# Optimization experiments

Hardware: AMD Instinct MI355X
Metric: run time of the kernel (lower is better)

The kernel has to match this reference:

```python
import jax, jax.numpy as jnp
import numpy as np
import math

# --- config (matches init_kwargs) ---
C = 128          # sphere_channels (multiplicity per l)
LMAX = 2
H = 8            # attention heads
B = 16           # graphs per batch (uniform)
M = 512          # nodes per graph
N = B * M        # 8192 nodes
E = 262144       # edges
D = C * sum(2 * l + 1 for l in range(LMAX + 1))  # 1152
_INV_SQRT_C = 1.0 / math.sqrt(C)


def irreps_linear(x, W):
    """e3nn o3.Linear irreps_node->irreps_node: per-l channel mixing, shared over m.
    x: [N, D], W: [LMAX+1, C, C]."""
    outs = []
    s = 0
    for l in range(LMAX + 1):
        d = 2 * l + 1
        blk = x[:, s:s + C * d].reshape(-1, C, d)          # [N, C, 2l+1]
        y = jnp.einsum('ncm,oc->nom', blk, W[l]) * _INV_SQRT_C
        outs.append(y.reshape(-1, C * d))
        s += C * d
    return jnp.concatenate(outs, axis=1)


def init_edge_rot_mat(edge_vec, edge_rand):
    """Faithful port of init_edge_rot_mat; edge_rand plays the role of rand_like."""
    dist = jnp.sqrt(jnp.sum(edge_vec ** 2, axis=1, keepdims=True))
    nx_ = edge_vec / dist
    e2 = edge_rand - 0.5
    e2 = e2 / jnp.sqrt(jnp.sum(e2 ** 2, axis=1, keepdims=True))
    e2b = jnp.stack([-e2[:, 1], e2[:, 0], e2[:, 2]], axis=1)
    e2c = jnp.stack([e2[:, 0], -e2[:, 2], e2[:, 1]], axis=1)
    dot = lambda a: jnp.abs(jnp.sum(a * nx_, axis=1, keepdims=True))
    vdb, vdc = dot(e2b), dot(e2c)
    e2 = jnp.where(dot(e2) > vdb, e2b, e2)
    e2 = jnp.where(dot(e2) > vdc, e2c, e2)
    nz = jnp.cross(nx_, e2)
    nz = nz / jnp.sqrt(jnp.sum(nz ** 2, axis=1, keepdims=True))
    ny = jnp.cross(nx_, nz)
    ny = ny / jnp.sqrt(jnp.sum(ny ** 2, axis=1, keepdims=True))
    rot_inv = jnp.stack([nz, nx_, -ny], axis=2)  # columns [z, x, -y]
    return jnp.transpose(rot_inv, (0, 2, 1))     # [E, 3, 3]


def setup_inputs() -> dict:
    key = jax.random.key(0)
    ks = jax.random.split(key, 10)
    node_features = jax.random.normal(ks[0], (N, D), dtype=jnp.float32)
    edge_vec = jax.random.normal(ks[1], (E, 3), dtype=jnp.float32)
    edge_rand = jax.random.uniform(ks[2], (E, 3), dtype=jnp.float32)
    edge_index = jax.random.randint(ks[3], (2, E), 0, N, dtype=jnp.int32)
    batch = jnp.repeat(jnp.arange(B, dtype=jnp.int32), M)
    W_q = jax.random.normal(ks[4], (LMAX + 1, C, C), dtype=jnp.float32)
    W_k = jax.random.normal(ks[5], (LMAX + 1, C, C), dtype=jnp.float32)
    W_v = jax.random.normal(ks[6], (LMAX + 1, C, C), dtype=jnp.float32)
    W_o = jax.random.normal(ks[7], (LMAX + 1, C, C), dtype=jnp.float32)
    gamma = jnp.ones((C,), dtype=jnp.float32)
    beta = jnp.zeros((C,), dtype=jnp.float32)
    return dict(node_features=node_features, edge_vec=edge_vec, edge_rand=edge_rand,
                W_q=W_q, W_k=W_k, W_v=W_v, W_o=W_o, gamma=gamma, beta=beta,
                edge_index=edge_index, batch=batch)


def reference(node_features, edge_vec, edge_rand, W_q, W_k, W_v, W_o, gamma, beta,
              edge_index, batch):
    # 1) per-edge rotation matrices (detached in the original)
    rot = jax.lax.stop_gradient(init_edge_rot_mat(edge_vec, edge_rand))

    x = node_features  # [N, D] equivariant irreps features

    # 2) SO2EquivariantGraphAttention: irreps q/k/v, dense per-graph multi-head attn
    q = irreps_linear(x, W_q)
    k = irreps_linear(x, W_k)
    v = irreps_linear(x, W_v)
    hd = D // H
    scale = 1.0 / math.sqrt(hd)
    # to_dense_batch with uniform graph sizes == reshape; mask all-true
    qd = q.reshape(B, M, H, hd).transpose(0, 2, 1, 3)  # [B,H,M,hd]
    kd = k.reshape(B, M, H, hd).transpose(0, 2, 1, 3)
    vd = v.reshape(B, M, H, hd).transpose(0, 2, 1, 3)
    scores = jnp.einsum('bhqd,bhkd->bhqk', qd, kd) * scale
    attn_w = jax.nn.softmax(scores, axis=-1)
    o = jnp.einsum('bhqk,bhkd->bhqd', attn_w, vd)
    o = o.transpose(0, 2, 1, 3).reshape(N, D)
    attn_out = irreps_linear(o, W_o)

    # residual connection
    x = x + attn_out

    # 3) EquivariantLayerNormV2: LayerNorm over l=0 dims only (first C)
    inv = x[:, :C]
    mu = jnp.mean(inv, axis=-1, keepdims=True)
    var = jnp.var(inv, axis=-1, keepdims=True)
    inv = (inv - mu) / jnp.sqrt(var + 1e-5) * gamma + beta

    # 4) S2Activation: SiLU on scalar (l=0) components, identity elsewhere
    inv = jax.nn.silu(inv)
    out = jnp.concatenate([inv, x[:, C:]], axis=1)
    return out, rot
```

## Files before the change

kernel.cpp:

```cpp
#include <hip/hip_runtime.h>
#include <hip/hip_bf16.h>

#define C_CH   128
#define DROW   1152
#define NNODE  8192
#define BATCH  16
#define MSEQ   512
#define NHEAD  8
#define HD     144
#define NEDGE  262144

typedef unsigned short ushort_t;
typedef __attribute__((ext_vector_type(8))) short bf16x8;
typedef __attribute__((ext_vector_type(4))) float f32x4;

__device__ __forceinline__ ushort_t f2bu(float x) {
    __hip_bfloat16 h = __float2bfloat16(x);
    return *reinterpret_cast<ushort_t*>(&h);
}
__device__ __forceinline__ float bu2f(ushort_t u) {
    return __bfloat162float(*reinterpret_cast<__hip_bfloat16*>(&u));
}
__device__ __forceinline__ unsigned u16of(const uint4 v, int ii) {
    const unsigned w = ((ii >> 1) == 0) ? v.x : ((ii >> 1) == 1) ? v.y :
                       ((ii >> 1) == 2) ? v.z : v.w;
    return (ii & 1) ? (w >> 16) : (w & 0xFFFFu);
}

#define KP2 136

template<int DL, int NPB, typename TX, typename TY>
__global__ __launch_bounds__(256) void lin_ovl(
    const TX* __restrict__ X,
    const float* __restrict__ W0, const float* __restrict__ W1,
    const float* __restrict__ W2,
    TY* __restrict__ Y0, TY* __restrict__ Y1, TY* __restrict__ Y2,
    const float* __restrict__ resid,
    int baseoff)
{
    constexpr int COLS = NPB * DL;
    constexpr int CT   = COLS / 16;
    __shared__ __align__(16) ushort_t Bs[COLS][KP2];

    const int tid  = threadIdx.x;
    const int wave = tid >> 6;
    const int lane = tid & 63;
    const int l15  = lane & 15;
    const int quad = lane >> 4;
    const int n0   = blockIdx.x * NPB;
    const int z    = blockIdx.y;

    const float* W = (z == 0) ? W0 : (z == 1 ? W1 : W2);
    TY* Y          = (z == 0) ? Y0 : (z == 1 ? Y1 : Y2);

    if constexpr (sizeof(TX) == 4) {
        for (int e4 = tid; e4 < NPB * 32 * DL; e4 += 256) {
            const int nb = e4 / (32 * DL);
            const int rr = (e4 - nb * (32 * DL)) * 4;
            const float4 xv = *reinterpret_cast<const float4*>(
                &X[(size_t)(n0 + nb) * DROW + baseoff + rr]);
            #pragma unroll
            for (int j = 0; j < 4; ++j) {
                const int r = rr + j, c = r / DL, m = r - c * DL;
                Bs[nb * DL + m][c] = f2bu(reinterpret_cast<const float*>(&xv)[j]);
            }
        }
    } else {
        for (int e8 = tid; e8 < NPB * 16 * DL; e8 += 256) {
            const int nb = e8 / (16 * DL);
            const int rr = (e8 - nb * (16 * DL)) * 8;
            const uint4 xv = *reinterpret_cast<const uint4*>(
                &X[(size_t)(n0 + nb) * DROW + baseoff + rr]);
            const ushort_t* xs = reinterpret_cast<const ushort_t*>(&xv);
            #pragma unroll
            for (int j = 0; j < 8; ++j) {
                const int r = rr + j, c = r / DL, m = r - c * DL;
                Bs[nb * DL + m][c] = xs[j];
            }
        }
    }

    const float s = 0.08838834764831845f;

    bf16x8 aw[2][4];
    #pragma unroll
    for (int ot = 0; ot < 2; ++ot)
        #pragma unroll
        for (int kst = 0; kst < 4; ++kst) {
            const float* wp = &W[(size_t)(32 * wave + 16 * ot + l15) * 128 + kst * 32 + quad * 8];
            const float4 wa = *reinterpret_cast<const float4*>(wp);
            const float4 wb = *reinterpret_cast<const float4*>(wp + 4);
            ushort_t t[8] = {f2bu(wa.x), f2bu(wa.y), f2bu(wa.z), f2bu(wa.w),
                             f2bu(wb.x), f2bu(wb.y), f2bu(wb.z), f2bu(wb.w)};
            aw[ot][kst] = *reinterpret_cast<const bf16x8*>(t);
        }

    __syncthreads();

    f32x4 acc[CT][2];
    #pragma unroll
    for (int ct = 0; ct < CT; ++ct) {
        acc[ct][0] = (f32x4){0.f, 0.f, 0.f, 0.f};
        acc[ct][1] = (f32x4){0.f, 0.f, 0.f, 0.f};
    }
    #pragma unroll
    for (int kst = 0; kst < 4; ++kst)
        #pragma unroll
        for (int ct = 0; ct < CT; ++ct) {
            const bf16x8 b = *reinterpret_cast<const bf16x8*>(
                &Bs[ct * 16 + l15][kst * 32 + quad * 8]);
            acc[ct][0] = __builtin_amdgcn_mfma_f32_16x16x32_bf16(aw[0][kst], b, acc[ct][0], 0, 0, 0);
            acc[ct][1] = __builtin_amdgcn_mfma_f32_16x16x32_bf16(aw[1][kst], b, acc[ct][1], 0, 0, 0);
        }

    __syncthreads();

    #pragma unroll
    for (int ct = 0; ct < CT; ++ct)
        #pragma unroll
        for (int ot = 0; ot < 2; ++ot) {
            ushort_t t[4] = {f2bu(acc[ct][ot][0] * s), f2bu(acc[ct][ot][1] * s),
                             f2bu(acc[ct][ot][2] * s), f2bu(acc[ct][ot][3] * s)};
            *reinterpret_cast<uint2*>(&Bs[ct * 16 + l15][32 * wave + 16 * ot + quad * 4]) =
                *reinterpret_cast<const uint2*>(t);
        }
    __syncthreads();

    for (int e8 = tid; e8 < COLS * 16; e8 += 256) {
        const int nb = e8 / (16 * DL);
        const int r0 = (e8 - nb * (16 * DL)) * 8;
        const size_t ga = (size_t)(n0 + nb) * DROW + baseoff + r0;
        if constexpr (sizeof(TY) == 2) {
            ushort_t t[8];
            #pragma unroll
            for (int j = 0; j < 8; ++j) {
                const int r = r0 + j;
                t[j] = Bs[nb * DL + r % DL][r / DL];
            }
            *reinterpret_cast<uint4*>(&Y[ga]) = *reinterpret_cast<const uint4*>(t);
        } else {
            #pragma unroll
            for (int j4 = 0; j4 < 2; ++j4) {
                const float4 rv = *reinterpret_cast<const float4*>(&resid[ga + j4 * 4]);
                float4 ov;
                #pragma unroll
                for (int j = 0; j < 4; ++j) {
                    const int r = r0 + j4 * 4 + j;
                    reinterpret_cast<float*>(&ov)[j] =
                        bu2f(Bs[nb * DL + r % DL][r / DL]) +
                        reinterpret_cast<const float*>(&rv)[j];
                }
                *reinterpret_cast<float4*>(&((float*)Y)[ga + j4 * 4]) = ov;
            }
        }
    }
}

template<int DL, int NPB, int NZ, int FUSE_LN, typename TX, typename TY>
__global__ __launch_bounds__(256) void lin_mfma(
    const TX* __restrict__ X,
    const float* __restrict__ W0, const float* __restrict__ W1,
    const float* __restrict__ W2,
    TY* __restrict__ Y0, TY* __restrict__ Y1, TY* __restrict__ Y2,
    const float* __restrict__ resid,
    const float* __restrict__ gamma, const float* __restrict__ beta,
    int baseoff)
{
    constexpr int COLS = NPB * DL;
    constexpr int CT   = COLS / 16;
    __shared__ __align__(16) ushort_t Xs[COLS][KP2];
    __shared__ __align__(16) ushort_t Es[COLS][KP2];

    const int tid  = threadIdx.x;
    const int wave = tid >> 6;
    const int lane = tid & 63;
    const int l15  = lane & 15;
    const int quad = lane >> 4;
    const int n0   = blockIdx.x * NPB;

    if constexpr (sizeof(TX) == 4) {
        for (int e4 = tid; e4 < NPB * 32 * DL; e4 += 256) {
            const int nb = e4 / (32 * DL);
            const int rr = (e4 - nb * (32 * DL)) * 4;
            const float4 xv = *reinterpret_cast<const float4*>(
                &X[(size_t)(n0 + nb) * DROW + baseoff + rr]);
            #pragma unroll
            for (int j = 0; j < 4; ++j) {
                const int r = rr + j, c = r / DL, m = r - c * DL;
                Xs[nb * DL + m][c] = f2bu(reinterpret_cast<const float*>(&xv)[j]);
            }
        }
    } else {
        for (int e8 = tid; e8 < NPB * 16 * DL; e8 += 256) {
            const int nb = e8 / (16 * DL);
            const int rr = (e8 - nb * (16 * DL)) * 8;
            const uint4 xv = *reinterpret_cast<const uint4*>(
                &X[(size_t)(n0 + nb) * DROW + baseoff + rr]);
            const ushort_t* xs = reinterpret_cast<const ushort_t*>(&xv);
            #pragma unroll
            for (int j = 0; j < 8; ++j) {
                const int r = rr + j, c = r / DL, m = r - c * DL;
                Xs[nb * DL + m][c] = xs[j];
            }
        }
    }

    const float s = 0.08838834764831845f;

    for (int z = 0; z < NZ; ++z) {
        const float* W = (z == 0) ? W0 : (z == 1 ? W1 : W2);
        TY* Y          = (z == 0) ? Y0 : (z == 1 ? Y1 : Y2);

        bf16x8 aw[2][4];
        #pragma unroll
        for (int ot = 0; ot < 2; ++ot)
            #pragma unroll
            for (int kst = 0; kst < 4; ++kst) {
                const float* wp = &W[(size_t)(32 * wave + 16 * ot + l15) * 128 + kst * 32 + quad * 8];
                const float4 wa = *reinterpret_cast<const float4*>(wp);
                const float4 wb = *reinterpret_cast<const float4*>(wp + 4);
                ushort_t t[8] = {f2bu(wa.x), f2bu(wa.y), f2bu(wa.z), f2bu(wa.w),
                                 f2bu(wb.x), f2bu(wb.y), f2bu(wb.z), f2bu(wb.w)};
                aw[ot][kst] = *reinterpret_cast<const bf16x8*>(t);
            }

        __syncthreads();

        f32x4 acc[CT][2];
        #pragma unroll
        for (int ct = 0; ct < CT; ++ct) {
            acc[ct][0] = (f32x4){0.f, 0.f, 0.f, 0.f};
            acc[ct][1] = (f32x4){0.f, 0.f, 0.f, 0.f};
        }
        #pragma unroll
        for (int kst = 0; kst < 4; ++kst)
            #pragma unroll
            for (int ct = 0; ct < CT; ++ct) {
                const bf16x8 b = *reinterpret_cast<const bf16x8*>(
                    &Xs[ct * 16 + l15][kst * 32 + quad * 8]);
                acc[ct][0] = __builtin_amdgcn_mfma_f32_16x16x32_bf16(aw[0][kst], b, acc[ct][0], 0, 0, 0);
                acc[ct][1] = __builtin_amdgcn_mfma_f32_16x16x32_bf16(aw[1][kst], b, acc[ct][1], 0, 0, 0);
            }

        #pragma unroll
        for (int ct = 0; ct < CT; ++ct)
            #pragma unroll
            for (int ot = 0; ot < 2; ++ot) {
                ushort_t t[4] = {f2bu(acc[ct][ot][0] * s), f2bu(acc[ct][ot][1] * s),
                                 f2bu(acc[ct][ot][2] * s), f2bu(acc[ct][ot][3] * s)};
                *reinterpret_cast<uint2*>(&Es[ct * 16 + l15][32 * wave + 16 * ot + quad * 4]) =
                    *reinterpret_cast<const uint2*>(t);
            }
        __syncthreads();

        if constexpr (FUSE_LN) {
            if (tid < NPB * 4) {
                const int nb = tid >> 2, cc = tid & 3;
                float y[32];
                const float* xr = resid + (size_t)(n0 + nb) * DROW + cc * 32;
                float s1 = 0.f, s2 = 0.f;
                #pragma unroll
                for (int j4 = 0; j4 < 8; ++j4) {
                    const float4 rv = *reinterpret_cast<const float4*>(xr + j4 * 4);
                    #pragma unroll
                    for (int j = 0; j < 4; ++j) {
                        const float v = bu2f(Es[nb][cc * 32 + j4 * 4 + j]) +
                                        reinterpret_cast<const float*>(&rv)[j];
                        y[j4 * 4 + j] = v; s1 += v; s2 += v * v;
                    }
                }
                s1 += __shfl_xor(s1, 1); s2 += __shfl_xor(s2, 1);
                s1 += __shfl_xor(s1, 2); s2 += __shfl_xor(s2, 2);
                const float mean = s1 * (1.0f / 128.0f);
                const float var  = s2 * (1.0f / 128.0f) - mean * mean;
                const float rstd = rsqrtf(var + 1e-5f);
                float* op = (float*)Y + (size_t)(n0 + nb) * DROW + cc * 32;
                #pragma unroll
                for (int j4 = 0; j4 < 8; ++j4) {
                    float4 ov;
                    #pragma unroll
                    for (int j = 0; j < 4; ++j) {
                        const int c = cc * 32 + j4 * 4 + j;
                        float t = (y[j4 * 4 + j] - mean) * rstd * gamma[c] + beta[c];
                        reinterpret_cast<float*>(&ov)[j] = t / (1.0f + __expf(-t));
                    }
                    *reinterpret_cast<float4*>(op + j4 * 4) = ov;
                }
            }
        } else {
            for (int e8 = tid; e8 < COLS * 16; e8 += 256) {
                const int nb = e8 / (16 * DL);
                const int r0 = (e8 - nb * (16 * DL)) * 8;
                const size_t ga = (size_t)(n0 + nb) * DROW + baseoff + r0;
                if constexpr (sizeof(TY) == 2) {
                    ushort_t t[8];
                    #pragma unroll
                    for (int j = 0; j < 8; ++j) {
                        const int r = r0 + j;
                        t[j] = Es[nb * DL + r % DL][r / DL];
                    }
                    *reinterpret_cast<uint4*>(&Y[ga]) = *reinterpret_cast<const uint4*>(t);
                } else {
                    #pragma unroll
                    for (int j4 = 0; j4 < 2; ++j4) {
                        const float4 rv = *reinterpret_cast<const float4*>(&resid[ga + j4 * 4]);
                        float4 ov;
                        #pragma unroll
                        for (int j = 0; j < 4; ++j) {
                            const int r = r0 + j4 * 4 + j;
                            reinterpret_cast<float*>(&ov)[j] =
                                bu2f(Es[nb * DL + r % DL][r / DL]) +
                                reinterpret_cast<const float*>(&rv)[j];
                        }
                        *reinterpret_cast<float4*>(&((float*)Y)[ga + j4 * 4]) = ov;
                    }
                }
            }
        }
    }
}

#define KPAD  168
#define VROWS 160
#define VPAD2 72
#define PPAD  68

__global__ __launch_bounds__(256, 2) void attn_kernel(
    const __hip_bfloat16* __restrict__ Q, const __hip_bfloat16* __restrict__ K,
    const __hip_bfloat16* __restrict__ V, __hip_bfloat16* __restrict__ O)
{
    __shared__ __align__(16) ushort_t ksqs[64][KPAD];
    __shared__ __align__(16) ushort_t vst[VROWS][VPAD2];
    __shared__ __align__(16) ushort_t ps[128][PPAD];

    const int tid  = threadIdx.x;
    const int wave = tid >> 6;
    const int lane = tid & 63;
    const int l15  = lane & 15;
    const int quad = lane >> 4;

    const int bid = blockIdx.x;
    const int xcd = bid & 7;
    const int j   = bid >> 3;
    const int bh  = xcd * 16 + (j >> 2);
    const int q0  = (j & 3) * 128;
    const int h   = bh & 7;
    const int b   = bh >> 3;
    const size_t rowbase = (size_t)b * MSEQ * DROW + (size_t)h * HD;
    const float EXSCALE = 0.12022458674074695f;

    const int r0 = tid / 18,          g0 = tid % 18;
    const int r1 = (tid + 256) / 18,  g1 = (tid + 256) % 18;
    const int r2 = (tid + 512) / 18,  g2 = (tid + 512) % 18;
    const int r3 = (tid + 768) / 18,  g3 = (tid + 768) % 18;
    const int r4 = (tid + 1024) / 18, g4 = (tid + 1024) % 18;
    const int ko0 = r0 * DROW + g0 * 8, ko1 = r1 * DROW + g1 * 8;
    const int ko2 = r2 * DROW + g2 * 8, ko3 = r3 * DROW + g3 * 8;
    const int ko4 = r4 * DROW + g4 * 8;
    ushort_t* kld0 = &ksqs[r0][g0 * 8];
    ushort_t* kld1 = &ksqs[r1][g1 * 8];
    ushort_t* kld2 = &ksqs[r2][g2 * 8];
    ushort_t* kld3 = &ksqs[r3][g3 * 8];
    ushort_t* kld4 = &ksqs[r4][g4 * 8];
    const int rqa = tid / 18,          ga = tid % 18;
    const int rqb = (tid + 256) / 18,  gb = (tid + 256) % 18;
    const int voa = (rqa * 4) * DROW + ga * 8;
    const int vob = (rqb * 4) * DROW + gb * 8;
    const int vca = 4 * (rqa ^ ((ga & 3) << 2));
    const int vcb = 4 * (rqb ^ ((gb & 3) << 2));
    const bool hasK4 = (tid < 128);
    const bool hasVB = (tid < 32);

    uint4 kp0, kp1, kp2, kp3, kp4;
    uint4 va0, va1, va2, va3, vb0, vb1, vb2, vb3;

#define LOAD_K(KC) do { \
        const __hip_bfloat16* kb_ = K + rowbase + (size_t)((KC) * 64) * DROW; \
        kp0 = *reinterpret_cast<const uint4*>(kb_ + ko0); \
        kp1 = *reinterpret_cast<const uint4*>(kb_ + ko1); \
        kp2 = *reinterpret_cast<const uint4*>(kb_ + ko2); \
        kp3 = *reinterpret_cast<const uint4*>(kb_ + ko3); \
        if (hasK4) kp4 = *reinterpret_cast<const uint4*>(kb_ + ko4); \
    } while (0)

#define LOAD_V(KC) do { \
        const __hip_bfloat16* vbp_ = V + rowbase + (size_t)((KC) * 64) * DROW; \
        va0 = *reinterpret_cast<const uint4*>(vbp_ + voa); \
        va1 = *reinterpret_cast<const uint4*>(vbp_ + voa + DROW); \
        va2 = *reinterpret_cast<const uint4*>(vbp_ + voa + 2 * DROW); \
        va3 = *reinterpret_cast<const uint4*>(vbp_ + voa + 3 * DROW); \
        if (hasVB) { \
            vb0 = *reinterpret_cast<const uint4*>(vbp_ + vob); \
            vb1 = *reinterpret_cast<const uint4*>(vbp_ + vob + DROW); \
            vb2 = *reinterpret_cast<const uint4*>(vbp_ + vob + 2 * DROW); \
            vb3 = *reinterpret_cast<const uint4*>(vbp_ + vob + 3 * DROW); \
        } \
    } while (0)

#define WRITE_KV() do { \
        *reinterpret_cast<uint4*>(kld0) = kp0; \
        *reinterpret_cast<uint4*>(kld1) = kp1; \
        *reinterpret_cast<uint4*>(kld2) = kp2; \
        *reinterpret_cast<uint4*>(kld3) = kp3; \
        if (hasK4) *reinterpret_cast<uint4*>(kld4) = kp4; \
        _Pragma("unroll") \
        for (int ii = 0; ii < 8; ++ii) { \
            uint2 pk; \
            pk.x = u16of(va0, ii) | (u16of(va1, ii) << 16); \
            pk.y = u16of(va2, ii) | (u16of(va3, ii) << 16); \
            *reinterpret_cast<uint2*>(&vst[ga * 8 + ii][vca]) = pk; \
        } \
        if (hasVB) { \
            _Pragma("unroll") \
            for (int ii = 0; ii < 8; ++ii) { \
                uint2 pk; \
                pk.x = u16of(vb0, ii) | (u16of(vb1, ii) << 16); \
                pk.y = u16of(vb2, ii) | (u16of(vb3, ii) << 16); \
                *reinterpret_cast<uint2*>(&vst[gb * 8 + ii][vcb]) = pk; \
            } \
        } \
    } while (0)

    LOAD_K(0);
    LOAD_V(0);

    for (int idx = tid; idx < 64 * 16; idx += 256)
        ksqs[idx >> 4][HD + (idx & 15)] = 0;
    for (int idx = tid; idx < 16 * VPAD2; idx += 256)
        vst[144 + idx / VPAD2][idx % VPAD2] = (idx / VPAD2 == 0) ? (ushort_t)0x3F80 : (ushort_t)0;

    bf16x8 aq[2][5];
    for (int hh = 0; hh < 2; ++hh) {
        __syncthreads();
        for (int idx = tid; idx < 64 * 18; idx += 256) {
            const int r = idx / 18, g = idx % 18;
            *reinterpret_cast<uint4*>(&ksqs[r][g * 8]) =
                *reinterpret_cast<const uint4*>(&Q[rowbase + (size_t)(q0 + hh * 64 + r) * DROW + g * 8]);
        }
        __syncthreads();
        if ((wave >> 1) == hh) {
            #pragma unroll
            for (int rt = 0; rt < 2; ++rt)
                #pragma unroll
                for (int kst = 0; kst < 5; ++kst)
                    aq[rt][kst] = *reinterpret_cast<const bf16x8*>(
                        &ksqs[32 * (wave & 1) + rt * 16 + l15][kst * 32 + quad * 8]);
        }
    }

    f32x4 oacc[2][10];
    #pragma unroll
    for (int rt = 0; rt < 2; ++rt)
        #pragma unroll
        for (int nt = 0; nt < 10; ++nt) oacc[rt][nt] = (f32x4){0.f, 0.f, 0.f, 0.f};

    for (int kc = 0; kc < 8; ++kc) {
        __syncthreads();
        WRITE_KV();
        __syncthreads();
        if (kc < 7) LOAD_K(kc + 1);

        f32x4 sc[2][4];
        #pragma unroll
        for (int rt = 0; rt < 2; ++rt)
            #pragma unroll
            for (int kt = 0; kt < 4; ++kt) sc[rt][kt] = (f32x4){0.f, 0.f, 0.f, 0.f};
        #pragma unroll
        for (int kst = 0; kst < 5; ++kst) {
            bf16x8 bk[4];
            #pragma unroll
            for (int kt = 0; kt < 4; ++kt)
                bk[kt] = *reinterpret_cast<const bf16x8*>(
                    &ksqs[kt * 16 + l15][kst * 32 + quad * 8]);
            #pragma unroll
            for (int rt = 0; rt < 2; ++rt)
                #pragma unroll
                for (int kt = 0; kt < 4; ++kt)
                    sc[rt][kt] = __builtin_amdgcn_mfma_f32_16x16x32_bf16(aq[rt][kst], bk[kt], sc[rt][kt], 0, 0, 0);
        }

        if (kc < 7) LOAD_V(kc + 1);

        #pragma unroll
        for (int rt = 0; rt < 2; ++rt)
            #pragma unroll
            for (int kt = 0; kt < 4; ++kt)
                #pragma unroll
                for (int i = 0; i < 4; ++i)
                    ps[32 * wave + 16 * rt + quad * 4 + i][16 * kt + l15] =
                        f2bu(exp2f(sc[rt][kt][i] * EXSCALE));

        #pragma unroll
        for (int kp = 0; kp < 2; ++kp) {
            bf16x8 pa[2];
            #pragma unroll
            for (int rt = 0; rt < 2; ++rt)
                pa[rt] = *reinterpret_cast<const bf16x8*>(
                    &ps[32 * wave + 16 * rt + l15][kp * 32 + quad * 8]);
            #pragma unroll
            for (int nt = 0; nt < 10; ++nt) {
                const int vrow = nt * 16 + l15;
                const int vcol = 4 * ((kp * 8 + quad * 2) ^ (((vrow >> 3) & 3) << 2));
                const bf16x8 bv = *reinterpret_cast<const bf16x8*>(&vst[vrow][vcol]);
                #pragma unroll
                for (int rt = 0; rt < 2; ++rt)
                    oacc[rt][nt] = __builtin_amdgcn_mfma_f32_16x16x32_bf16(pa[rt], bv, oacc[rt][nt], 0, 0, 0);
            }
        }
    }

    #pragma unroll
    for (int rt = 0; rt < 2; ++rt) {
        #pragma unroll
        for (int i = 0; i < 4; ++i) {
            const float l = __shfl(oacc[rt][9][i], lane & 48);
            const float inv = 1.0f / l;
            const int row = q0 + 32 * wave + 16 * rt + quad * 4 + i;
            const size_t rb = rowbase + (size_t)row * DROW;
            #pragma unroll
            for (int nt = 0; nt < 9; ++nt)
                O[rb + nt * 16 + l15] = __float2bfloat16(oacc[rt][nt][i] * inv);
        }
    }
#undef LOAD_K
#undef LOAD_V
#undef WRITE_KV
}

#define ROT_BLOCKS  (NEDGE / 256)
#define CONV_BLOCKS 1152

__global__ __launch_bounds__(256) void rot_conv_kernel(
    const float* __restrict__ ev, const float* __restrict__ er,
    float* __restrict__ rot,
    const float* __restrict__ x, __hip_bfloat16* __restrict__ xb)
{
    const int bx = blockIdx.x;
    if (bx >= ROT_BLOCKS) {
        const int t = (bx - ROT_BLOCKS) * 256 + threadIdx.x;
        const float4* X4 = reinterpret_cast<const float4*>(x);
        uint2* XB2 = reinterpret_cast<uint2*>(xb);
        const int NV4 = NNODE * DROW / 4;
        const int NTH = CONV_BLOCKS * 256;
        #pragma unroll
        for (int it = 0; it < 8; ++it) {
            const int i = t + it * NTH;
            (void)NV4;
            const float4 v = X4[i];
            uint2 o;
            o.x = (unsigned)f2bu(v.x) | ((unsigned)f2bu(v.y) << 16);
            o.y = (unsigned)f2bu(v.z) | ((unsigned)f2bu(v.w) << 16);
            XB2[i] = o;
        }
        return;
    }
    const int e = bx * 256 + threadIdx.x;
    if (e >= NEDGE) return;
    const float vx = ev[e * 3 + 0], vy = ev[e * 3 + 1], vz = ev[e * 3 + 2];
    const float d = sqrtf(vx * vx + vy * vy + vz * vz);
    const float nx0 = vx / d, nx1 = vy / d, nx2 = vz / d;
    float r0 = er[e * 3 + 0] - 0.5f;
    float r1 = er[e * 3 + 1] - 0.5f;
    float r2 = er[e * 3 + 2] - 0.5f;
    const float rn = sqrtf(r0 * r0 + r1 * r1 + r2 * r2);
    r0 /= rn; r1 /= rn; r2 /= rn;
    const float b0 = -r1, b1 = r0, b2v = r2;
    const float c0 = r0, c1 = -r2, c2 = r1;
    const float vd0 = fabsf(r0 * nx0 + r1 * nx1 + r2 * nx2);
    const float vdb = fabsf(b0 * nx0 + b1 * nx1 + b2v * nx2);
    const float vdc = fabsf(c0 * nx0 + c1 * nx1 + c2 * nx2);
    if (vd0 > vdb) { r0 = b0; r1 = b1; r2 = b2v; }
    const float vd1 = fabsf(r0 * nx0 + r1 * nx1 + r2 * nx2);
    if (vd1 > vdc) { r0 = c0; r1 = c1; r2 = c2; }
    float z0 = nx1 * r2 - nx2 * r1;
    float z1 = nx2 * r0 - nx0 * r2;
    float z2 = nx0 * r1 - nx1 * r0;
    const float zn = sqrtf(z0 * z0 + z1 * z1 + z2 * z2);
    z0 /= zn; z1 /= zn; z2 /= zn;
    float y0 = nx1 * z2 - nx2 * z1;
    float y1 = nx2 * z0 - nx0 * z2;
    float y2 = nx0 * z1 - nx1 * z0;
    const float yn = sqrtf(y0 * y0 + y1 * y1 + y2 * y2);
    y0 /= yn; y1 /= yn; y2 /= yn;
    float* rp = rot + (size_t)e * 9;
    rp[0] = z0;   rp[1] = z1;   rp[2] = z2;
    rp[3] = nx0;  rp[4] = nx1;  rp[5] = nx2;
    rp[6] = -y0;  rp[7] = -y1;  rp[8] = -y2;
}

extern "C" void kernel_launch(void* const* d_in, const int* in_sizes, int n_in,
                              void* d_out, int out_size, void* d_ws, size_t ws_size,
                              hipStream_t stream)
{
    (void)in_sizes; (void)n_in; (void)out_size; (void)ws_size;
    const float* x     = (const float*)d_in[0];
    const float* ev    = (const float*)d_in[1];
    const float* er    = (const float*)d_in[2];
    const float* Wq    = (const float*)d_in[3];
    const float* Wk    = (const float*)d_in[4];
    const float* Wv    = (const float*)d_in[5];
    const float* Wo    = (const float*)d_in[6];
    const float* gamma = (const float*)d_in[7];
    const float* beta  = (const float*)d_in[8];

    float* out = (float*)d_out;
    float* rot = out + (size_t)NNODE * DROW;

    const size_t ND = (size_t)NNODE * DROW;
    __hip_bfloat16* q = (__hip_bfloat16*)d_ws;
    __hip_bfloat16* k = q + ND;
    __hip_bfloat16* v = k + ND;
    __hip_bfloat16* o = v + ND;
    __hip_bfloat16* xb = o;

    rot_conv_kernel<<<ROT_BLOCKS + CONV_BLOCKS, 256, 0, stream>>>(
        ev, er, rot, x, xb);

    lin_ovl<1, 32, __hip_bfloat16, __hip_bfloat16><<<dim3(NNODE / 32, 3), 256, 0, stream>>>(
        xb, Wq, Wk, Wv, q, k, v, nullptr, 0);
    lin_ovl<3, 16, __hip_bfloat16, __hip_bfloat16><<<dim3(NNODE / 16, 3), 256, 0, stream>>>(
        xb, Wq + 16384, Wk + 16384, Wv + 16384, q, k, v, nullptr, 128);
    lin_ovl<5, 16, __hip_bfloat16, __hip_bfloat16><<<dim3(NNODE / 16, 3), 256, 0, stream>>>(
        xb, Wq + 32768, Wk + 32768, Wv + 32768, q, k, v, nullptr, 512);

    attn_kernel<<<(MSEQ / 128) * NHEAD * BATCH, 256, 0, stream>>>(q, k, v, o);

    lin_mfma<1, 32, 1, 1, __hip_bfloat16, float><<<NNODE / 32, 256, 0, stream>>>(
        o, Wo, nullptr, nullptr, out, nullptr, nullptr, x, gamma, beta, 0);
    lin_ovl<3, 16, __hip_bfloat16, float><<<dim3(NNODE / 16, 1), 256, 0, stream>>>(
        o, Wo + 16384, nullptr, nullptr, out, nullptr, nullptr, x, 128);
    lin_ovl<5, 16, __hip_bfloat16, float><<<dim3(NNODE / 16, 1), 256, 0, stream>>>(
        o, Wo + 32768, nullptr, nullptr, out, nullptr, nullptr, x, 512);
}
```

Measured before the change: 235.0 us.

## Fuse per-l irreps linear launches into single QKV and output-projection kernels

Replaces three separate per-l QKV projection launches with one kernel that loads whole node rows (l=0,1,2) into shared memory once and runs all three weight blocks over them. Likewise merges the l=1 and l=2 output-projection launches into one kernel with a fused residual add. This cuts launch count and makes node-row reads and writes contiguous over the full row, at the cost of more accumulator registers (18 f32x4) and more complex index remapping per element.

```diff
diff --git a/kernel.cpp b/kernel.cpp
--- a/kernel.cpp
+++ b/kernel.cpp
@@ -29,94 +29,89 @@
 
 #define KP2 136
 
-template<int DL, int NPB, typename TX, typename TY>
-__global__ __launch_bounds__(256) void lin_ovl(
-    const TX* __restrict__ X,
-    const float* __restrict__ W0, const float* __restrict__ W1,
-    const float* __restrict__ W2,
-    TY* __restrict__ Y0, TY* __restrict__ Y1, TY* __restrict__ Y2,
-    const float* __restrict__ resid,
-    int baseoff)
+__global__ __launch_bounds__(256) void qkv_fused2(
+    const __hip_bfloat16* __restrict__ X,
+    const float* __restrict__ Wq, const float* __restrict__ Wk,
+    const float* __restrict__ Wv,
+    __hip_bfloat16* __restrict__ Yq, __hip_bfloat16* __restrict__ Yk,
+    __hip_bfloat16* __restrict__ Yv)
 {
-    constexpr int COLS = NPB * DL;
-    constexpr int CT   = COLS / 16;
-    __shared__ __align__(16) ushort_t Bs[COLS][KP2];
+    __shared__ __align__(16) ushort_t Bs[144][KP2];
 
     const int tid  = threadIdx.x;
     const int wave = tid >> 6;
     const int lane = tid & 63;
     const int l15  = lane & 15;
     const int quad = lane >> 4;
-    const int n0   = blockIdx.x * NPB;
+    const int n0   = blockIdx.x * 16;
     const int z    = blockIdx.y;
 
-    const float* W = (z == 0) ? W0 : (z == 1 ? W1 : W2);
-    TY* Y          = (z == 0) ? Y0 : (z == 1 ? Y1 : Y2);
-
-    if constexpr (sizeof(TX) == 4) {
-        for (int e4 = tid; e4 < NPB * 32 * DL; e4 += 256) {
-            const int nb = e4 / (32 * DL);
-            const int rr = (e4 - nb * (32 * DL)) * 4;
-            const float4 xv = *reinterpret_cast<const float4*>(
-                &X[(size_t)(n0 + nb) * DROW + baseoff + rr]);
-            #pragma unroll
-            for (int j = 0; j < 4; ++j) {
-                const int r = rr + j, c = r / DL, m = r - c * DL;
-                Bs[nb * DL + m][c] = f2bu(reinterpret_cast<const float*>(&xv)[j]);
-            }
-        }
-    } else {
-        for (int e8 = tid; e8 < NPB * 16 * DL; e8 += 256) {
-            const int nb = e8 / (16 * DL);
-            const int rr = (e8 - nb * (16 * DL)) * 8;
-            const uint4 xv = *reinterpret_cast<const uint4*>(
-                &X[(size_t)(n0 + nb) * DROW + baseoff + rr]);
-            const ushort_t* xs = reinterpret_cast<const ushort_t*>(&xv);
-            #pragma unroll
-            for (int j = 0; j < 8; ++j) {
-                const int r = rr + j, c = r / DL, m = r - c * DL;
-                Bs[nb * DL + m][c] = xs[j];
-            }
+    const float* Wz   = (z == 0) ? Wq : (z == 1 ? Wk : Wv);
+    __hip_bfloat16* Y = (z == 0) ? Yq : (z == 1 ? Yk : Yv);
+
+    for (int e8 = tid; e8 < 16 * 144; e8 += 256) {
+        const int nb = e8 / 144;
+        const int rr = (e8 - nb * 144) * 8;
+        const uint4 xv = *reinterpret_cast<const uint4*>(
+            &X[(size_t)(n0 + nb) * DROW + rr]);
+        const ushort_t* xs = reinterpret_cast<const ushort_t*>(&xv);
+        #pragma unroll
+        for (int j = 0; j < 8; ++j) {
+            const int r = rr + j;
+            int col, c;
+            if (r < 128)      { col = nb; c = r; }
+            else if (r < 512) { const int t = r - 128; c = t / 3; col = 16 + nb * 3 + (t - c * 3); }
+            else              { const int t = r - 512; c = t / 5; col = 64 + nb * 5 + (t - c * 5); }
+            Bs[col][c] = xs[j];
         }
     }
 
     const float s = 0.08838834764831845f;
 
-    bf16x8 aw[2][4];
+    __syncthreads();
+
+    f32x4 acc[9][2];
     #pragma unroll
-    for (int ot = 0; ot < 2; ++ot)
-        #pragma unroll
-        for (int kst = 0; kst < 4; ++kst) {
-            const float* wp = &W[(size_t)(32 * wave + 16 * ot + l15) * 128 + kst * 32 + quad * 8];
-            const float4 wa = *reinterpret_cast<const float4*>(wp);
-            const float4 wb = *reinterpret_cast<const float4*>(wp + 4);
-            ushort_t t[8] = {f2bu(wa.x), f2bu(wa.y), f2bu(wa.z), f2bu(wa.w),
-                             f2bu(wb.x), f2bu(wb.y), f2bu(wb.z), f2bu(wb.w)};
-            aw[ot][kst] = *reinterpret_cast<const bf16x8*>(t);
-        }
-
-    __syncthreads();
-
-    f32x4 acc[CT][2];
-    #pragma unroll
-    for (int ct = 0; ct < CT; ++ct) {
+    for (int ct = 0; ct < 9; ++ct) {
         acc[ct][0] = (f32x4){0.f, 0.f, 0.f, 0.f};
         acc[ct][1] = (f32x4){0.f, 0.f, 0.f, 0.f};
     }
+
     #pragma unroll
-    for (int kst = 0; kst < 4; ++kst)
-        #pragma unroll
-        for (int ct = 0; ct < CT; ++ct) {
-            const bf16x8 b = *reinterpret_cast<const bf16x8*>(
-                &Bs[ct * 16 + l15][kst * 32 + quad * 8]);
-            acc[ct][0] = __builtin_amdgcn_mfma_f32_16x16x32_bf16(aw[0][kst], b, acc[ct][0], 0, 0, 0);
-            acc[ct][1] = __builtin_amdgcn_mfma_f32_16x16x32_bf16(aw[1][kst], b, acc[ct][1], 0, 0, 0);
-        }
+    for (int lg = 0; lg < 3; ++lg) {
+        const int woff = lg * 16384;
+        const int ctlo = (lg == 0) ? 0 : (lg == 1 ? 1 : 4);
+        const int cthi = (lg == 0) ? 1 : (lg == 1 ? 4 : 9);
+        const float* W = Wz + woff;
+
+        bf16x8 aw[2][4];
+        #pragma unroll
+        for (int ot = 0; ot < 2; ++ot)
+            #pragma unroll
+            for (int kst = 0; kst < 4; ++kst) {
+                const float* wp = &W[(size_t)(32 * wave + 16 * ot + l15) * 128 + kst * 32 + quad * 8];
+                const float4 wa = *reinterpret_cast<const float4*>(wp);
+                const float4 wb = *reinterpret_cast<const float4*>(wp + 4);
+                ushort_t t[8] = {f2bu(wa.x), f2bu(wa.y), f2bu(wa.z), f2bu(wa.w),
+                                 f2bu(wb.x), f2bu(wb.y), f2bu(wb.z), f2bu(wb.w)};
+                aw[ot][kst] = *reinterpret_cast<const bf16x8*>(t);
+            }
+
+        #pragma unroll
+        for (int kst = 0; kst < 4; ++kst)
+            #pragma unroll 9
+            for (int ct = ctlo; ct < cthi; ++ct) {
+                const bf16x8 b = *reinterpret_cast<const bf16x8*>(
+                    &Bs[ct * 16 + l15][kst * 32 + quad * 8]);
+                acc[ct][0] = __builtin_amdgcn_mfma_f32_16x16x32_bf16(aw[0][kst], b, acc[ct][0], 0, 0, 0);
+                acc[ct][1] = __builtin_amdgcn_mfma_f32_16x16x32_bf16(aw[1][kst], b, acc[ct][1], 0, 0, 0);
+            }
+    }
 
     __syncthreads();
 
     #pragma unroll
-    for (int ct = 0; ct < CT; ++ct)
+    for (int ct = 0; ct < 9; ++ct)
         #pragma unroll
         for (int ot = 0; ot < 2; ++ot) {
             ushort_t t[4] = {f2bu(acc[ct][ot][0] * s), f2bu(acc[ct][ot][1] * s),
@@ -126,32 +121,126 @@
         }
     __syncthreads();
 
-    for (int e8 = tid; e8 < COLS * 16; e8 += 256) {
-        const int nb = e8 / (16 * DL);
-        const int r0 = (e8 - nb * (16 * DL)) * 8;
-        const size_t ga = (size_t)(n0 + nb) * DROW + baseoff + r0;
-        if constexpr (sizeof(TY) == 2) {
-            ushort_t t[8];
-            #pragma unroll
-            for (int j = 0; j < 8; ++j) {
-                const int r = r0 + j;
-                t[j] = Bs[nb * DL + r % DL][r / DL];
-            }
-            *reinterpret_cast<uint4*>(&Y[ga]) = *reinterpret_cast<const uint4*>(t);
-        } else {
-            #pragma unroll
-            for (int j4 = 0; j4 < 2; ++j4) {
-                const float4 rv = *reinterpret_cast<const float4*>(&resid[ga + j4 * 4]);
-                float4 ov;
-                #pragma unroll
-                for (int j = 0; j < 4; ++j) {
-                    const int r = r0 + j4 * 4 + j;
-                    reinterpret_cast<float*>(&ov)[j] =
-                        bu2f(Bs[nb * DL + r % DL][r / DL]) +
-                        reinterpret_cast<const float*>(&rv)[j];
-                }
-                *reinterpret_cast<float4*>(&((float*)Y)[ga + j4 * 4]) = ov;
-            }
+    for (int e8 = tid; e8 < 16 * 144; e8 += 256) {
+        const int nb = e8 / 144;
+        const int rr = (e8 - nb * 144) * 8;
+        ushort_t t[8];
+        #pragma unroll
+        for (int j = 0; j < 8; ++j) {
+            const int r = rr + j;
+            int col, o;
+            if (r < 128)      { col = nb; o = r; }
+            else if (r < 512) { const int u = r - 128; o = u / 3; col = 16 + nb * 3 + (u - o * 3); }
+            else              { const int u = r - 512; o = u / 5; col = 64 + nb * 5 + (u - o * 5); }
+            t[j] = Bs[col][o];
+        }
+        *reinterpret_cast<uint4*>(&Y[(size_t)(n0 + nb) * DROW + rr]) =
+            *reinterpret_cast<const uint4*>(t);
+    }
+}
+
+__global__ __launch_bounds__(256) void out_l12(
+    const __hip_bfloat16* __restrict__ O, const float* __restrict__ Wo,
+    float* __restrict__ out, const float* __restrict__ resid)
+{
+    __shared__ __align__(16) ushort_t Bs[128][KP2];
+
+    const int tid  = threadIdx.x;
+    const int wave = tid >> 6;
+    const int lane = tid & 63;
+    const int l15  = lane & 15;
+    const int quad = lane >> 4;
+    const int n0   = blockIdx.x * 16;
+
+    for (int e8 = tid; e8 < 16 * 128; e8 += 256) {
+        const int nb = e8 / 128;
+        const int rr = 128 + (e8 - nb * 128) * 8;
+        const uint4 xv = *reinterpret_cast<const uint4*>(
+            &O[(size_t)(n0 + nb) * DROW + rr]);
+        const ushort_t* xs = reinterpret_cast<const ushort_t*>(&xv);
+        #pragma unroll
+        for (int j = 0; j < 8; ++j) {
+            const int r = rr + j;
+            int col, c;
+            if (r < 512) { const int t = r - 128; c = t / 3; col = nb * 3 + (t - c * 3); }
+            else         { const int t = r - 512; c = t / 5; col = 48 + nb * 5 + (t - c * 5); }
+            Bs[col][c] = xs[j];
+        }
+    }
+
+    const float s = 0.08838834764831845f;
+
+    __syncthreads();
+
+    f32x4 acc[8][2];
+    #pragma unroll
+    for (int ct = 0; ct < 8; ++ct) {
+        acc[ct][0] = (f32x4){0.f, 0.f, 0.f, 0.f};
+        acc[ct][1] = (f32x4){0.f, 0.f, 0.f, 0.f};
+    }
+
+    #pragma unroll
+    for (int lg = 0; lg < 2; ++lg) {
+        const int woff = (lg == 0) ? 16384 : 32768;
+        const int ctlo = (lg == 0) ? 0 : 3;
+        const int cthi = (lg == 0) ? 3 : 8;
+        const float* W = Wo + woff;
+
+        bf16x8 aw[2][4];
+        #pragma unroll
+        for (int ot = 0; ot < 2; ++ot)
+            #pragma unroll
+            for (int kst = 0; kst < 4; ++kst) {
+                const float* wp = &W[(size_t)(32 * wave + 16 * ot + l15) * 128 + kst * 32 + quad * 8];
+                const float4 wa = *reinterpret_cast<const float4*>(wp);
+                const float4 wb = *reinterpret_cast<const float4*>(wp + 4);
+                ushort_t t[8] = {f2bu(wa.x), f2bu(wa.y), f2bu(wa.z), f2bu(wa.w),
+                                 f2bu(wb.x), f2bu(wb.y), f2bu(wb.z), f2bu(wb.w)};
+                aw[ot][kst] = *reinterpret_cast<const bf16x8*>(t);
+            }
+
+        #pragma unroll
+        for (int kst = 0; kst < 4; ++kst)
+            #pragma unroll 8
+            for (int ct = ctlo; ct < cthi; ++ct) {
+                const bf16x8 b = *reinterpret_cast<const bf16x8*>(
+                    &Bs[ct * 16 + l15][kst * 32 + quad * 8]);
+                acc[ct][0] = __builtin_amdgcn_mfma_f32_16x16x32_bf16(aw[0][kst], b, acc[ct][0], 0, 0, 0);
+                acc[ct][1] = __builtin_amdgcn_mfma_f32_16x16x32_bf16(aw[1][kst], b, acc[ct][1], 0, 0, 0);
+            }
+    }
+
+    __syncthreads();
+
+    #pragma unroll
+    for (int ct = 0; ct < 8; ++ct)
+        #pragma unroll
+        for (int ot = 0; ot < 2; ++ot) {
+            ushort_t t[4] = {f2bu(acc[ct][ot][0] * s), f2bu(acc[ct][ot][1] * s),
+                             f2bu(acc[ct][ot][2] * s), f2bu(acc[ct][ot][3] * s)};
+            *reinterpret_cast<uint2*>(&Bs[ct * 16 + l15][32 * wave + 16 * ot + quad * 4]) =
+                *reinterpret_cast<const uint2*>(t);
+        }
+    __syncthreads();
+
+    for (int e8 = tid; e8 < 16 * 128; e8 += 256) {
+        const int nb = e8 / 128;
+        const int rr = 128 + (e8 - nb * 128) * 8;
+        const size_t ga = (size_t)(n0 + nb) * DROW + rr;
+        #pragma unroll
+        for (int j4 = 0; j4 < 2; ++j4) {
+            const float4 rv = *reinterpret_cast<const float4*>(&resid[ga + j4 * 4]);
+            float4 ov;
+            #pragma unroll
+            for (int j = 0; j < 4; ++j) {
+                const int r = rr + j4 * 4 + j;
+                int col, o;
+                if (r < 512) { const int t = r - 128; o = t / 3; col = nb * 3 + (t - o * 3); }
+                else         { const int t = r - 512; o = t / 5; col = 48 + nb * 5 + (t - o * 5); }
+                reinterpret_cast<float*>(&ov)[j] = bu2f(Bs[col][o]) +
+                    reinterpret_cast<const float*>(&rv)[j];
+            }
+            *reinterpret_cast<float4*>(&out[ga + j4 * 4]) = ov;
         }
     }
 }
@@ -540,12 +629,10 @@
         const int t = (bx - ROT_BLOCKS) * 256 + threadIdx.x;
         const float4* X4 = reinterpret_cast<const float4*>(x);
         uint2* XB2 = reinterpret_cast<uint2*>(xb);
-        const int NV4 = NNODE * DROW / 4;
         const int NTH = CONV_BLOCKS * 256;
         #pragma unroll
         for (int it = 0; it < 8; ++it) {
             const int i = t + it * NTH;
-            (void)NV4;
             const float4 v = X4[i];
             uint2 o;
             o.x = (unsigned)f2bu(v.x) | ((unsigned)f2bu(v.y) << 16);
@@ -616,19 +703,13 @@
     rot_conv_kernel<<<ROT_BLOCKS + CONV_BLOCKS, 256, 0, stream>>>(
         ev, er, rot, x, xb);
 
-    lin_ovl<1, 32, __hip_bfloat16, __hip_bfloat16><<<dim3(NNODE / 32, 3), 256, 0, stream>>>(
-        xb, Wq, Wk, Wv, q, k, v, nullptr, 0);
-    lin_ovl<3, 16, __hip_bfloat16, __hip_bfloat16><<<dim3(NNODE / 16, 3), 256, 0, stream>>>(
-        xb, Wq + 16384, Wk + 16384, Wv + 16384, q, k, v, nullptr, 128);
-    lin_ovl<5, 16, __hip_bfloat16, __hip_bfloat16><<<dim3(NNODE / 16, 3), 256, 0, stream>>>(
-        xb, Wq + 32768, Wk + 32768, Wv + 32768, q, k, v, nullptr, 512);
+    qkv_fused2<<<dim3(NNODE / 16, 3), 256, 0, stream>>>(
+        xb, Wq, Wk, Wv, q, k, v);
 
     attn_kernel<<<(MSEQ / 128) * NHEAD * BATCH, 256, 0, stream>>>(q, k, v, o);
 
     lin_mfma<1, 32, 1, 1, __hip_bfloat16, float><<<NNODE / 32, 256, 0, stream>>>(
         o, Wo, nullptr, nullptr, out, nullptr, nullptr, x, gamma, beta, 0);
-    lin_ovl<3, 16, __hip_bfloat16, float><<<dim3(NNODE / 16, 1), 256, 0, stream>>>(
-        o, Wo + 16384, nullptr, nullptr, out, nullptr, nullptr, x, 128);
-    lin_ovl<5, 16, __hip_bfloat16, float><<<dim3(NNODE / 16, 1), 256, 0, stream>>>(
-        o, Wo + 32768, nullptr, nullptr, out, nullptr, nullptr, x, 512);
-}
+
+    out_l12<<<NNODE / 16, 256, 0, stream>>>(o, Wo, out, x);
+}
```

After: 255.4 us. +8.7%, slower.
